# Performance work log

Measured on AMD Instinct MI355X. Metric: run time of the kernel, lower is better.

The kernel has to match this reference:

```python
import jax, jax.numpy as jnp
import numpy as np

NUM_HEADS = 8


def setup_inputs() -> dict:
    key = jax.random.key(0)
    ks = jax.random.split(key, 6)
    B, C, H, W = 64, 512, 16, 16
    x = jax.random.normal(ks[0], (B, C, H, W), dtype=jnp.float32)
    qkv_w = jax.random.normal(ks[1], (3 * C, C), dtype=jnp.float32) * (C ** -0.5)
    qkv_b = jax.random.normal(ks[2], (3 * C,), dtype=jnp.float32) * 0.02
    out_w = jax.random.normal(ks[3], (C, C), dtype=jnp.float32) * (C ** -0.5)
    out_b = jax.random.normal(ks[4], (C,), dtype=jnp.float32) * 0.02
    rel_pos_enc = jax.random.normal(ks[5], (NUM_HEADS, 2 * 16 - 1, 2 * 16 - 1), dtype=jnp.float32) * 0.02
    return {"x": x, "qkv_w": qkv_w, "qkv_b": qkv_b, "out_w": out_w,
            "out_b": out_b, "rel_pos_enc": rel_pos_enc}


def _attention(x, qkv_w, qkv_b, out_w, out_b, rel_pos_enc):
    B, C, H, W = x.shape
    heads = rel_pos_enc.shape[0]
    hd = C // heads
    N = H * W

    # 1x1 conv qkv projection == pointwise GEMM over channels
    qkv = jnp.einsum('bchw,oc->bohw', x, qkv_w) + qkv_b[None, :, None, None]
    q, k, v = jnp.split(qkv, 3, axis=1)  # each (B, C, H, W)
    q = q.reshape(B, heads, hd, N)
    k = k.reshape(B, heads, hd, N)
    v = v.reshape(B, heads, hd, N)

    attn = jnp.einsum('bhdn,bhdm->bhnm', q, k) * (hd ** -0.5)  # (B,h,N,N)

    # gathered 2D relative position bias: bias[head,(h1,w1),(h2,w2)] =
    #   rel_pos_enc[head, h1-h2+15, w1-w2+15]
    h_idx = (jnp.arange(H)[:, None] - jnp.arange(H)[None, :]) + 16 - 1  # (H,H)
    w_idx = (jnp.arange(W)[:, None] - jnp.arange(W)[None, :]) + 16 - 1  # (W,W)
    bias = rel_pos_enc[:, h_idx[:, None, :, None], w_idx[None, :, None, :]]  # (h,H,W,H,W)
    bias = bias.reshape(heads, N, N)

    attn = jax.nn.softmax(attn + bias[None], axis=-1)
    out = jnp.einsum('bhnm,bhdm->bhdn', attn, v).reshape(B, C, H, W)
    out = jnp.einsum('bchw,oc->bohw', out, out_w) + out_b[None, :, None, None]
    return out


def reference(x, qkv_w, qkv_b, out_w, out_b, rel_pos_enc):
    return _attention(x, qkv_w, qkv_b, out_w, out_b, rel_pos_enc)
```

## Files before the change

### kernel.cpp

```cpp
#include <hip/hip_runtime.h>

typedef __attribute__((ext_vector_type(8))) short short8;
typedef __attribute__((ext_vector_type(4))) float floatx4;

#define MFMA16(a,b,c) __builtin_amdgcn_mfma_f32_16x16x32_bf16((a),(b),(c),0,0,0)

static __device__ __forceinline__ unsigned short f2bf(float f){
    unsigned int u = __float_as_uint(f);
    u = (u + 0x7FFFu + ((u >> 16) & 1u)) >> 16;
    return (unsigned short)u;
}

static __device__ __forceinline__ void async16(const unsigned short* g, const unsigned short* l){
    __builtin_amdgcn_global_load_lds(
        (const __attribute__((address_space(1))) unsigned int*)g,
        (__attribute__((address_space(3))) unsigned int*)l, 16, 0, 0);
}

__global__ __launch_bounds__(256) void k_prep(const float* __restrict__ x,
                                              unsigned short* __restrict__ xT,
                                              const float* __restrict__ qkvw,
                                              unsigned short* __restrict__ wqkv,
                                              const float* __restrict__ outw,
                                              unsigned short* __restrict__ wout){
    __shared__ unsigned short tile[64][72];
    const int bid = blockIdx.x;
    const int tid = threadIdx.x;
    if (bid < 2048){
        const int c0 = (bid & 7) * 64;
        const int n0 = ((bid >> 3) & 3) * 64;
        const int b  = bid >> 5;
        const int chunk = tid & 7;
        const int r     = tid >> 3;
        const float*    src = x  + (size_t)b * 131072;
        unsigned short* dst = xT + (size_t)b * 131072;
#pragma unroll
        for (int it = 0; it < 2; ++it){
            int c = r + it * 32;
            const float* p = src + (size_t)(c0 + c) * 256 + n0 + chunk * 8;
            float4 f0 = *(const float4*)(p);
            float4 f1 = *(const float4*)(p + 4);
            short8 v;
            v[0]=(short)f2bf(f0.x); v[1]=(short)f2bf(f0.y); v[2]=(short)f2bf(f0.z); v[3]=(short)f2bf(f0.w);
            v[4]=(short)f2bf(f1.x); v[5]=(short)f2bf(f1.y); v[6]=(short)f2bf(f1.z); v[7]=(short)f2bf(f1.w);
            *(short8*)&tile[c][chunk * 8] = v;
        }
        __syncthreads();
#pragma unroll
        for (int it = 0; it < 2; ++it){
            int n = r + it * 32;
            short8 o;
#pragma unroll
            for (int e = 0; e < 8; ++e) o[e] = (short)tile[chunk * 8 + e][n];
            *(short8*)(dst + (size_t)(n0 + n) * 512 + c0 + chunk * 8) = o;
        }
    } else {
        int i = (bid - 2048) * 256 + tid;
        const float* s; unsigned short* d; int j;
        if (i < 196608){ s = qkvw; d = wqkv; j = i; }
        else { j = i - 196608; if (j >= 65536) return; s = outw; d = wout; }
        float4 f = *(const float4*)(s + (size_t)j * 4);
        uint2 v;
        v.x = (unsigned int)f2bf(f.x) | ((unsigned int)f2bf(f.y) << 16);
        v.y = (unsigned int)f2bf(f.z) | ((unsigned int)f2bf(f.w) << 16);
        *(uint2*)(d + (size_t)j * 4) = v;
    }
}

__global__ __launch_bounds__(512, 2) void k_fused(const unsigned short* __restrict__ xT,
                                                  const unsigned short* __restrict__ wbf,
                                                  const float* __restrict__ qkvb,
                                                  const float* __restrict__ rel,
                                                  unsigned short* __restrict__ ao){
    __shared__ unsigned short SH[79748];
    const int XS = 0;
    const int WS = 16384;
    const int QS = 28672;
    const int KS = 45056;
    const int VS = 61440;
    float* Relsh = (float*)&SH[77824];

    const int bid  = blockIdx.x;
    const int xcd  = bid & 7;
    const int slot = bid >> 3;
    const int b = xcd * 8 + (slot & 7);
    const int h = slot >> 3;
    const int tid  = threadIdx.x;
    const int wave = tid >> 6;
    const int lane = tid & 63;
    const int lrow = lane & 15;
    const int lgrp = lane >> 4;
    const int mq = wave >> 1;
    const int nh = wave & 1;

    for (int i = tid; i < 961; i += 512) Relsh[i] = rel[h * 961 + i];

    floatx4 acc[4][6];
#pragma unroll
    for (int i = 0; i < 4; ++i)
#pragma unroll
        for (int j = 0; j < 6; ++j){ floatx4 z = {0.f,0.f,0.f,0.f}; acc[i][j] = z; }

    const unsigned short* xb = xT + (size_t)(b * 256) * 512;
    const unsigned short* xsrc[4]; const unsigned short* xdst[4];
#pragma unroll
    for (int c = 0; c < 4; ++c){
        int s   = (c * 8 + wave) * 64 + lane;
        int row = s >> 3, pch = s & 7;
        int sch = pch ^ (row & 7);
        xsrc[c] = xb + (size_t)row * 512 + sch * 8;
        xdst[c] = &SH[XS + (c * 8 + wave) * 512];
    }
    const unsigned short* wsrc[3]; const unsigned short* wdst[3];
#pragma unroll
    for (int c = 0; c < 3; ++c){
        int s   = (c * 8 + wave) * 64 + lane;
        int row = s >> 3, pch = s & 7;
        int sch = pch ^ (row & 7);
        int grow = (row >> 6) * 512 + h * 64 + (row & 63);
        wsrc[c] = wbf + (size_t)grow * 512 + sch * 8;
        wdst[c] = &SH[WS + (c * 8 + wave) * 512];
    }

    for (int kk = 0; kk < 512; kk += 64){
#pragma unroll
        for (int c = 0; c < 4; ++c) async16(xsrc[c] + kk, xdst[c]);
#pragma unroll
        for (int c = 0; c < 3; ++c) async16(wsrc[c] + kk, wdst[c]);
        __syncthreads();
#pragma unroll
        for (int ks = 0; ks < 2; ++ks){
            short8 af[4], bf[6];
#pragma unroll
            for (int mt = 0; mt < 4; ++mt){
                int row = mq * 64 + mt * 16 + lrow;
                int pch = (ks * 4 + lgrp) ^ (row & 7);
                af[mt] = *(const short8*)&SH[XS + row * 64 + pch * 8];
            }
#pragma unroll
            for (int nt = 0; nt < 6; ++nt){
                int row = nh * 96 + nt * 16 + lrow;
                int pch = (ks * 4 + lgrp) ^ (row & 7);
                bf[nt] = *(const short8*)&SH[WS + row * 64 + pch * 8];
            }
#pragma unroll
            for (int mt = 0; mt < 4; ++mt)
#pragma unroll
                for (int nt = 0; nt < 6; ++nt)
                    acc[mt][nt] = MFMA16(af[mt], bf[nt], acc[mt][nt]);
        }
        __syncthreads();
    }

#pragma unroll
    for (int mt = 0; mt < 4; ++mt){
#pragma unroll
        for (int nt = 0; nt < 6; ++nt){
            int col = nh * 96 + nt * 16 + lrow;
            int seg = col >> 6, off = col & 63;
            float bv = qkvb[seg * 512 + h * 64 + off];
#pragma unroll
            for (int r = 0; r < 4; ++r){
                int token = mq * 64 + mt * 16 + lgrp * 4 + r;
                unsigned short v = f2bf(acc[mt][nt][r] + bv);
                if (seg == 2){
                    int lch = token >> 3;
                    int pch = (lch & 24) | ((lch & 7) ^ (off & 7));
                    SH[VS + off * 256 + pch * 8 + (token & 7)] = v;
                } else {
                    int base = seg ? KS : QS;
                    int pch  = (off >> 3) ^ (token & 7);
                    SH[base + token * 64 + pch * 8 + (off & 7)] = v;
                }
            }
        }
    }
    __syncthreads();

    short8 aq[2][2];
#pragma unroll
    for (int pp = 0; pp < 2; ++pp)
#pragma unroll
        for (int kc = 0; kc < 2; ++kc){
            int row = wave * 32 + pp * 16 + lrow;
            int pch = (kc * 4 + lgrp) ^ (row & 7);
            aq[pp][kc] = *(const short8*)&SH[QS + row * 64 + pch * 8];
        }

    floatx4 s2[2][16];
#pragma unroll
    for (int pp = 0; pp < 2; ++pp)
#pragma unroll
        for (int ct = 0; ct < 16; ++ct){
            int row = ct * 16 + lrow;
            int pch0 = lgrp ^ (row & 7);
            short8 b0 = *(const short8*)&SH[KS + row * 64 + pch0 * 8];
            short8 b1 = *(const short8*)&SH[KS + row * 64 + (pch0 ^ 4) * 8];
            floatx4 z = {0.f,0.f,0.f,0.f};
            z = MFMA16(aq[pp][0], b0, z);
            z = MFMA16(aq[pp][1], b1, z);
            s2[pp][ct] = z;
        }

    float inv[2][4];
#pragma unroll
    for (int pp = 0; pp < 2; ++pp)
#pragma unroll
        for (int r = 0; r < 4; ++r){
            int n   = wave * 32 + pp * 16 + lgrp * 4 + r;
            int nh_ = n >> 4, nw = n & 15;
            float sum = 0.f;
#pragma unroll
            for (int ct = 0; ct < 16; ++ct){
                float e = __expf(s2[pp][ct][r] * 0.125f +
                                 Relsh[(nh_ - ct + 15) * 31 + (nw - lrow + 15)]);
                s2[pp][ct][r] = e;
                sum += e;
            }
#pragma unroll
            for (int off = 1; off < 16; off <<= 1)
                sum += __shfl_xor(sum, off, 64);
            inv[pp][r] = 1.f / sum;
        }

    __syncthreads();

    const int PB = QS + wave * 4096;
    unsigned short* aob = ao + (size_t)(b * 256) * 512 + h * 64;
#pragma unroll
    for (int pp = 0; pp < 2; ++pp){
#pragma unroll
        for (int ct = 0; ct < 16; ++ct)
#pragma unroll
            for (int r = 0; r < 4; ++r){
                int row = lgrp * 4 + r;
                int lch = ct * 2 + (lrow >> 3);
                int pch = (lch & 24) | ((lch & 7) ^ (row & 7));
                SH[PB + row * 256 + pch * 8 + (lrow & 7)] = f2bf(s2[pp][ct][r]);
            }
        short8 pa[8];
#pragma unroll
        for (int ms = 0; ms < 8; ++ms){
            int lch = ms * 4 + lgrp;
            int pch = (lch & 24) | ((lch & 7) ^ (lrow & 7));
            pa[ms] = *(const short8*)&SH[PB + lrow * 256 + pch * 8];
        }
#pragma unroll
        for (int dt = 0; dt < 4; ++dt){
            floatx4 accO = {0.f,0.f,0.f,0.f};
#pragma unroll
            for (int ms = 0; ms < 8; ++ms){
                int row = dt * 16 + lrow;
                int lch = ms * 4 + lgrp;
                int pch = (lch & 24) | ((lch & 7) ^ (row & 7));
                short8 vb = *(const short8*)&SH[VS + row * 256 + pch * 8];
                accO = MFMA16(pa[ms], vb, accO);
            }
#pragma unroll
            for (int r = 0; r < 4; ++r){
                int n = wave * 32 + pp * 16 + lgrp * 4 + r;
                aob[(size_t)n * 512 + dt * 16 + lrow] = f2bf(accO[r] * inv[pp][r]);
            }
        }
    }
}

__global__ __launch_bounds__(256, 2) void k_out(const unsigned short* __restrict__ ao,
                                                const unsigned short* __restrict__ wbf,
                                                const float* __restrict__ bias,
                                                float* __restrict__ out){
    __shared__ unsigned short Ash[2][128][32];
    __shared__ unsigned short Bsh[2][128][32];
    const int bid  = blockIdx.x;
    const int xcd  = bid & 7;
    const int slot = bid >> 3;
    const int t0 = (xcd * 16 + (slot & 15)) * 128;
    const int o0 = (slot >> 4) * 128;
    const int tid  = threadIdx.x;
    const int wave = tid >> 6;
    const int lane = tid & 63;
    const int lrow = lane & 15;
    const int lk8  = (lane >> 4) * 8;
    const int wm   = (wave >> 1) * 64;
    const int wn   = (wave & 1) * 64;
    const int ld_row = wave * 32 + (lane >> 2);
    const int ld_col = (lane & 3) * 8;

    floatx4 acc[4][4];
#pragma unroll
    for (int i = 0; i < 4; ++i)
#pragma unroll
        for (int j = 0; j < 4; ++j){ floatx4 z = {0.f,0.f,0.f,0.f}; acc[i][j] = z; }

    const unsigned short* gA = wbf + (size_t)(o0 + ld_row) * 512 + ld_col;
    const unsigned short* gB = ao  + (size_t)(t0 + ld_row) * 512 + ld_col;

    for (int kk = 0; kk < 512; kk += 64){
        async16(gA + kk,                 &Ash[0][wave * 32][0]);
        async16(gA + kk + 16 * 512,      &Ash[0][wave * 32 + 16][0]);
        async16(gA + kk + 32,            &Ash[1][wave * 32][0]);
        async16(gA + kk + 32 + 16 * 512, &Ash[1][wave * 32 + 16][0]);
        async16(gB + kk,                 &Bsh[0][wave * 32][0]);
        async16(gB + kk + 16 * 512,      &Bsh[0][wave * 32 + 16][0]);
        async16(gB + kk + 32,            &Bsh[1][wave * 32][0]);
        async16(gB + kk + 32 + 16 * 512, &Bsh[1][wave * 32 + 16][0]);
        __syncthreads();
#pragma unroll
        for (int s = 0; s < 2; ++s){
            short8 af[4], bf[4];
#pragma unroll
            for (int mt = 0; mt < 4; ++mt) af[mt] = *(const short8*)&Ash[s][wm + mt*16 + lrow][lk8];
#pragma unroll
            for (int nt = 0; nt < 4; ++nt) bf[nt] = *(const short8*)&Bsh[s][wn + nt*16 + lrow][lk8];
#pragma unroll
            for (int mt = 0; mt < 4; ++mt)
#pragma unroll
                for (int nt = 0; nt < 4; ++nt)
                    acc[mt][nt] = MFMA16(af[mt], bf[nt], acc[mt][nt]);
        }
        __syncthreads();
    }
#pragma unroll
    for (int mt = 0; mt < 4; ++mt){
        int orow0 = o0 + wm + mt*16 + (lane >> 4) * 4;
#pragma unroll
        for (int nt = 0; nt < 4; ++nt){
            int tcol = t0 + wn + nt*16 + lrow;
            int bb = tcol >> 8, nn = tcol & 255;
#pragma unroll
            for (int r = 0; r < 4; ++r){
                float bv = bias[orow0 + r];
                out[(size_t)(bb * 512 + orow0 + r) * 256 + nn] = acc[mt][nt][r] + bv;
            }
        }
    }
}

extern "C" void kernel_launch(void* const* d_in, const int* in_sizes, int n_in,
                              void* d_out, int out_size, void* d_ws, size_t ws_size,
                              hipStream_t stream){
    const float* x    = (const float*)d_in[0];
    const float* qkvw = (const float*)d_in[1];
    const float* qkvb = (const float*)d_in[2];
    const float* outw = (const float*)d_in[3];
    const float* outb = (const float*)d_in[4];
    const float* rel  = (const float*)d_in[5];
    float* out = (float*)d_out;

    const size_t XT_OFF = 0;
    const size_t AO_OFF = 16777216;
    const size_t W_OFF  = 33554432;
    const size_t NEED   = W_OFF + 4194304;
    if (ws_size < NEED) return;

    char* ws = (char*)d_ws;
    unsigned short* xT = (unsigned short*)(ws + XT_OFF);
    unsigned short* ao = (unsigned short*)(ws + AO_OFF);
    unsigned short* wqkv_bf = (unsigned short*)(ws + W_OFF);
    unsigned short* wout_bf = (unsigned short*)(ws + W_OFF + 2097152);

    hipLaunchKernelGGL(k_prep,  dim3(3072), dim3(256), 0, stream,
                       x, xT, qkvw, wqkv_bf, outw, wout_bf);
    hipLaunchKernelGGL(k_fused, dim3(512),  dim3(512), 0, stream,
                       xT, wqkv_bf, qkvb, rel, ao);
    hipLaunchKernelGGL(k_out,   dim3(512),  dim3(256), 0, stream,
                       ao, wout_bf, outb, out);
}
```

Before: 162.4 us.

## Double the K-tile depth in both GEMMs and alias fused-kernel LDS regions

```diff
diff --git a/kernel.cpp b/kernel.cpp
--- a/kernel.cpp
+++ b/kernel.cpp
@@ -1,6 +1,7 @@
 #include <hip/hip_runtime.h>
 
 typedef __attribute__((ext_vector_type(8))) short short8;
+typedef __attribute__((ext_vector_type(4))) short short4v;
 typedef __attribute__((ext_vector_type(4))) float floatx4;
 
 #define MFMA16(a,b,c) __builtin_amdgcn_mfma_f32_16x16x32_bf16((a),(b),(c),0,0,0)
@@ -72,13 +73,10 @@
                                                   const float* __restrict__ qkvb,
                                                   const float* __restrict__ rel,
                                                   unsigned short* __restrict__ ao){
-    __shared__ unsigned short SH[79748];
-    const int XS = 0;
-    const int WS = 16384;
-    const int QS = 28672;
-    const int KS = 45056;
-    const int VS = 61440;
-    float* Relsh = (float*)&SH[77824];
+    __shared__ unsigned short SH[59266];
+    const int XS = 0, WS = 32768;
+    const int QS = 0, KS = 16384, VS = 32768;
+    float* Relsh = (float*)&SH[57344];
 
     const int bid  = blockIdx.x;
     const int xcd  = bid & 7;
@@ -93,7 +91,7 @@
     const int mq = wave >> 1;
     const int nh = wave & 1;
 
-    for (int i = tid; i < 961; i += 512) Relsh[i] = rel[h * 961 + i];
+    for (int i = tid; i < 961; i += 512) Relsh[i] = rel[h * 961 + i] * 1.44269504f;
 
     floatx4 acc[4][6];
 #pragma unroll
@@ -102,46 +100,48 @@
         for (int j = 0; j < 6; ++j){ floatx4 z = {0.f,0.f,0.f,0.f}; acc[i][j] = z; }
 
     const unsigned short* xb = xT + (size_t)(b * 256) * 512;
-    const unsigned short* xsrc[4]; const unsigned short* xdst[4];
-#pragma unroll
-    for (int c = 0; c < 4; ++c){
+    int xoff[8], xdst[8];
+#pragma unroll
+    for (int c = 0; c < 8; ++c){
         int s   = (c * 8 + wave) * 64 + lane;
-        int row = s >> 3, pch = s & 7;
-        int sch = pch ^ (row & 7);
-        xsrc[c] = xb + (size_t)row * 512 + sch * 8;
-        xdst[c] = &SH[XS + (c * 8 + wave) * 512];
-    }
-    const unsigned short* wsrc[3]; const unsigned short* wdst[3];
-#pragma unroll
-    for (int c = 0; c < 3; ++c){
+        int row = s >> 4, pch = s & 15;
+        int sch = (pch & 8) | ((pch & 7) ^ (row & 7));
+        xoff[c] = row * 512 + sch * 8;
+        xdst[c] = XS + (c * 8 + wave) * 512;
+    }
+    int woff[6], wdst[6];
+#pragma unroll
+    for (int c = 0; c < 6; ++c){
         int s   = (c * 8 + wave) * 64 + lane;
-        int row = s >> 3, pch = s & 7;
-        int sch = pch ^ (row & 7);
+        int row = s >> 4, pch = s & 15;
+        int sch = (pch & 8) | ((pch & 7) ^ (row & 7));
         int grow = (row >> 6) * 512 + h * 64 + (row & 63);
-        wsrc[c] = wbf + (size_t)grow * 512 + sch * 8;
-        wdst[c] = &SH[WS + (c * 8 + wave) * 512];
-    }
-
-    for (int kk = 0; kk < 512; kk += 64){
-#pragma unroll
-        for (int c = 0; c < 4; ++c) async16(xsrc[c] + kk, xdst[c]);
-#pragma unroll
-        for (int c = 0; c < 3; ++c) async16(wsrc[c] + kk, wdst[c]);
-        __syncthreads();
-#pragma unroll
-        for (int ks = 0; ks < 2; ++ks){
+        woff[c] = grow * 512 + sch * 8;
+        wdst[c] = WS + (c * 8 + wave) * 512;
+    }
+
+    for (int kk = 0; kk < 512; kk += 128){
+#pragma unroll
+        for (int c = 0; c < 8; ++c) async16(xb + xoff[c] + kk, &SH[xdst[c]]);
+#pragma unroll
+        for (int c = 0; c < 6; ++c) async16(wbf + woff[c] + kk, &SH[wdst[c]]);
+        __syncthreads();
+#pragma unroll
+        for (int ks = 0; ks < 4; ++ks){
             short8 af[4], bf[6];
 #pragma unroll
             for (int mt = 0; mt < 4; ++mt){
                 int row = mq * 64 + mt * 16 + lrow;
-                int pch = (ks * 4 + lgrp) ^ (row & 7);
-                af[mt] = *(const short8*)&SH[XS + row * 64 + pch * 8];
+                int idx = ks * 4 + lgrp;
+                int phys = (idx & 8) | ((idx & 7) ^ (row & 7));
+                af[mt] = *(const short8*)&SH[XS + row * 128 + phys * 8];
             }
 #pragma unroll
             for (int nt = 0; nt < 6; ++nt){
                 int row = nh * 96 + nt * 16 + lrow;
-                int pch = (ks * 4 + lgrp) ^ (row & 7);
-                bf[nt] = *(const short8*)&SH[WS + row * 64 + pch * 8];
+                int idx = ks * 4 + lgrp;
+                int phys = (idx & 8) | ((idx & 7) ^ (row & 7));
+                bf[nt] = *(const short8*)&SH[WS + row * 128 + phys * 8];
             }
 #pragma unroll
             for (int mt = 0; mt < 4; ++mt)
@@ -154,23 +154,26 @@
 
 #pragma unroll
     for (int mt = 0; mt < 4; ++mt){
+        int tk0 = mq * 64 + mt * 16 + lgrp * 4;
 #pragma unroll
         for (int nt = 0; nt < 6; ++nt){
             int col = nh * 96 + nt * 16 + lrow;
             int seg = col >> 6, off = col & 63;
             float bv = qkvb[seg * 512 + h * 64 + off];
-#pragma unroll
-            for (int r = 0; r < 4; ++r){
-                int token = mq * 64 + mt * 16 + lgrp * 4 + r;
-                unsigned short v = f2bf(acc[mt][nt][r] + bv);
-                if (seg == 2){
-                    int lch = token >> 3;
-                    int pch = (lch & 24) | ((lch & 7) ^ (off & 7));
-                    SH[VS + off * 256 + pch * 8 + (token & 7)] = v;
-                } else {
-                    int base = seg ? KS : QS;
-                    int pch  = (off >> 3) ^ (token & 7);
-                    SH[base + token * 64 + pch * 8 + (off & 7)] = v;
+            if (seg == 2){
+                int lch = tk0 >> 3;
+                int pch = (lch & 24) | ((lch & 7) ^ (off & 7));
+                short4v v4;
+#pragma unroll
+                for (int r = 0; r < 4; ++r) v4[r] = (short)f2bf(acc[mt][nt][r] + bv);
+                *(short4v*)&SH[VS + off * 256 + pch * 8 + (tk0 & 7)] = v4;
+            } else {
+                int base = seg ? KS : QS;
+#pragma unroll
+                for (int r = 0; r < 4; ++r){
+                    int token = tk0 + r;
+                    int pch = (off >> 3) ^ (token & 7);
+                    SH[base + token * 64 + pch * 8 + (off & 7)] = f2bf(acc[mt][nt][r] + bv);
                 }
             }
         }
@@ -189,18 +192,19 @@
 
     floatx4 s2[2][16];
 #pragma unroll
-    for (int pp = 0; pp < 2; ++pp)
-#pragma unroll
-        for (int ct = 0; ct < 16; ++ct){
-            int row = ct * 16 + lrow;
-            int pch0 = lgrp ^ (row & 7);
-            short8 b0 = *(const short8*)&SH[KS + row * 64 + pch0 * 8];
-            short8 b1 = *(const short8*)&SH[KS + row * 64 + (pch0 ^ 4) * 8];
-            floatx4 z = {0.f,0.f,0.f,0.f};
-            z = MFMA16(aq[pp][0], b0, z);
-            z = MFMA16(aq[pp][1], b1, z);
-            s2[pp][ct] = z;
-        }
+    for (int ct = 0; ct < 16; ++ct){
+        int row = ct * 16 + lrow;
+        int pch0 = lgrp ^ (row & 7);
+        short8 b0 = *(const short8*)&SH[KS + row * 64 + pch0 * 8];
+        short8 b1 = *(const short8*)&SH[KS + row * 64 + (pch0 ^ 4) * 8];
+        floatx4 z0 = {0.f,0.f,0.f,0.f}, z1 = {0.f,0.f,0.f,0.f};
+        z0 = MFMA16(aq[0][0], b0, z0);
+        z0 = MFMA16(aq[0][1], b1, z0);
+        z1 = MFMA16(aq[1][0], b0, z1);
+        z1 = MFMA16(aq[1][1], b1, z1);
+        s2[0][ct] = z0;
+        s2[1][ct] = z1;
+    }
 
     float inv[2][4];
 #pragma unroll
@@ -209,11 +213,11 @@
         for (int r = 0; r < 4; ++r){
             int n   = wave * 32 + pp * 16 + lgrp * 4 + r;
             int nh_ = n >> 4, nw = n & 15;
+            const float* rbase = Relsh + (nh_ + 15) * 31 + (nw - lrow + 15);
             float sum = 0.f;
 #pragma unroll
             for (int ct = 0; ct < 16; ++ct){
-                float e = __expf(s2[pp][ct][r] * 0.125f +
-                                 Relsh[(nh_ - ct + 15) * 31 + (nw - lrow + 15)]);
+                float e = exp2f(s2[pp][ct][r] * 0.18033688f + rbase[-ct * 31]);
                 s2[pp][ct][r] = e;
                 sum += e;
             }
@@ -269,8 +273,8 @@
                                                 const unsigned short* __restrict__ wbf,
                                                 const float* __restrict__ bias,
                                                 float* __restrict__ out){
-    __shared__ unsigned short Ash[2][128][32];
-    __shared__ unsigned short Bsh[2][128][32];
+    __shared__ unsigned short Ash[16384];
+    __shared__ unsigned short Bsh[16384];
     const int bid  = blockIdx.x;
     const int xcd  = bid & 7;
     const int slot = bid >> 3;
@@ -280,11 +284,20 @@
     const int wave = tid >> 6;
     const int lane = tid & 63;
     const int lrow = lane & 15;
-    const int lk8  = (lane >> 4) * 8;
+    const int lgrp = lane >> 4;
     const int wm   = (wave >> 1) * 64;
     const int wn   = (wave & 1) * 64;
-    const int ld_row = wave * 32 + (lane >> 2);
-    const int ld_col = (lane & 3) * 8;
+
+    int aoff[8], boff[8], dstoff[8];
+#pragma unroll
+    for (int c = 0; c < 8; ++c){
+        int s   = (c * 4 + wave) * 64 + lane;
+        int row = s >> 4, pch = s & 15;
+        int sch = (pch & 8) | ((pch & 7) ^ (row & 7));
+        aoff[c] = (o0 + row) * 512 + sch * 8;
+        boff[c] = (t0 + row) * 512 + sch * 8;
+        dstoff[c] = (c * 4 + wave) * 512;
+    }
 
     floatx4 acc[4][4];
 #pragma unroll
@@ -292,26 +305,29 @@
 #pragma unroll
         for (int j = 0; j < 4; ++j){ floatx4 z = {0.f,0.f,0.f,0.f}; acc[i][j] = z; }
 
-    const unsigned short* gA = wbf + (size_t)(o0 + ld_row) * 512 + ld_col;
-    const unsigned short* gB = ao  + (size_t)(t0 + ld_row) * 512 + ld_col;
-
-    for (int kk = 0; kk < 512; kk += 64){
-        async16(gA + kk,                 &Ash[0][wave * 32][0]);
-        async16(gA + kk + 16 * 512,      &Ash[0][wave * 32 + 16][0]);
-        async16(gA + kk + 32,            &Ash[1][wave * 32][0]);
-        async16(gA + kk + 32 + 16 * 512, &Ash[1][wave * 32 + 16][0]);
-        async16(gB + kk,                 &Bsh[0][wave * 32][0]);
-        async16(gB + kk + 16 * 512,      &Bsh[0][wave * 32 + 16][0]);
-        async16(gB + kk + 32,            &Bsh[1][wave * 32][0]);
-        async16(gB + kk + 32 + 16 * 512, &Bsh[1][wave * 32 + 16][0]);
-        __syncthreads();
-#pragma unroll
-        for (int s = 0; s < 2; ++s){
+    for (int kk = 0; kk < 512; kk += 128){
+#pragma unroll
+        for (int c = 0; c < 8; ++c) async16(wbf + aoff[c] + kk, &Ash[dstoff[c]]);
+#pragma unroll
+        for (int c = 0; c < 8; ++c) async16(ao  + boff[c] + kk, &Bsh[dstoff[c]]);
+        __syncthreads();
+#pragma unroll
+        for (int ks = 0; ks < 4; ++ks){
             short8 af[4], bf[4];
 #pragma unroll
-            for (int mt = 0; mt < 4; ++mt) af[mt] = *(const short8*)&Ash[s][wm + mt*16 + lrow][lk8];
-#pragma unroll
-            for (int nt = 0; nt < 4; ++nt) bf[nt] = *(const short8*)&Bsh[s][wn + nt*16 + lrow][lk8];
+            for (int mt = 0; mt < 4; ++mt){
+                int row = wm + mt * 16 + lrow;
+                int idx = ks * 4 + lgrp;
+                int phys = (idx & 8) | ((idx & 7) ^ (row & 7));
+                af[mt] = *(const short8*)&Ash[row * 128 + phys * 8];
+            }
+#pragma unroll
+            for (int nt = 0; nt < 4; ++nt){
+                int row = wn + nt * 16 + lrow;
+                int idx = ks * 4 + lgrp;
+                int phys = (idx & 8) | ((idx & 7) ^ (row & 7));
+                bf[nt] = *(const short8*)&Bsh[row * 128 + phys * 8];
+            }
 #pragma unroll
             for (int mt = 0; mt < 4; ++mt)
 #pragma unroll
@@ -322,7 +338,7 @@
     }
 #pragma unroll
     for (int mt = 0; mt < 4; ++mt){
-        int orow0 = o0 + wm + mt*16 + (lane >> 4) * 4;
+        int orow0 = o0 + wm + mt*16 + lgrp * 4;
 #pragma unroll
         for (int nt = 0; nt < 4; ++nt){
             int tcol = t0 + wn + nt*16 + lrow;
```

Result: no change. 163.3 us (+0.5%).
